# Optimization experiments

Measured on AMD Instinct MI355X. Metric: run time of the kernel, lower is better.

## Reference

```python
import jax, jax.numpy as jnp
import numpy as np

B, C, H, W = 8, 512, 64, 64
CI = C // 8  # inter_channels = 64


def setup_inputs() -> dict:
    key = jax.random.key(0)
    k = jax.random.split(key, 8)
    s = 0.02
    return {
        "x": jax.random.normal(k[0], (B, C, H, W), dtype=jnp.float32),
        "wq": jax.random.normal(k[1], (CI, C), dtype=jnp.float32) * s,
        "bq": jnp.zeros((CI,), dtype=jnp.float32),
        "wk": jax.random.normal(k[2], (CI, C), dtype=jnp.float32) * s,
        "bk": jnp.zeros((CI,), dtype=jnp.float32),
        "wv": jax.random.normal(k[3], (C, C), dtype=jnp.float32) * s,
        "bv": jnp.zeros((C,), dtype=jnp.float32),
        # original inits gamma to 0 (which kills attention branch); use a
        # nonzero value so the attention path contributes to output/grads
        "gamma": jax.random.normal(k[4], (1,), dtype=jnp.float32),
    }


def reference(x, wq, bq, wk, bk, wv, bv, gamma):
    b, c, h, w = x.shape
    n = h * w
    xf = x.reshape(b, c, n)  # (B, C, HW)
    # 1x1 convs == per-pixel linear layers
    q = jnp.einsum("oc,bcn->bon", wq, xf) + bq[None, :, None]  # (B, CI, HW)
    k_ = jnp.einsum("oc,bcn->bon", wk, xf) + bk[None, :, None]  # (B, CI, HW)
    v = jnp.einsum("oc,bcn->bon", wv, xf) + bv[None, :, None]  # (B, C, HW)
    # energy[b, i, j] = <q[:, i], k[:, j]>  -> softmax over j
    energy = jnp.einsum("bdn,bdm->bnm", q, k_)  # (B, HW, HW)
    attn = jax.nn.softmax(energy, axis=-1)
    # note: torch code does bmm(value, attention) -> out[:, c, j] = sum_i v[:, c, i] * attn[:, i, j]
    out = jnp.einsum("bci,bij->bcj", v, attn).reshape(b, c, h, w)
    return gamma[0] * out + x
```

## Files before the change

### kernel.cpp

```cpp
#include <hip/hip_runtime.h>
#include <hip/hip_bf16.h>

#define N_TOK 4096
#define CCH   512

using f32x4  = __attribute__((ext_vector_type(4))) float;
using f32x16 = __attribute__((ext_vector_type(16))) float;
using bf16x4 = __attribute__((ext_vector_type(4))) short;
using bf16x8 = __attribute__((ext_vector_type(8))) short;
using u32x4  = __attribute__((ext_vector_type(4))) unsigned int;

__device__ __forceinline__ short f2bf(float f) {
  __hip_bfloat16 h = __float2bfloat16(f);
  return __builtin_bit_cast(short, h);
}

__device__ __forceinline__ unsigned pkexp(float a, float b) {
  unsigned ua = __builtin_bit_cast(unsigned, __expf(a));
  unsigned ub = __builtin_bit_cast(unsigned, __expf(b));
  ua = ua + 0x7fffu + ((ua >> 16) & 1u);
  ub = ub + 0x7fffu + ((ub >> 16) & 1u);
  return (ua >> 16) | (ub & 0xffff0000u);
}

__device__ __forceinline__ f32x16 mfma32(bf16x8 a, bf16x8 b, f32x16 c) {
  return __builtin_amdgcn_mfma_f32_32x32x16_bf16(a, b, c, 0, 0, 0);
}

__device__ __forceinline__ void gload16(const void* g, void* l) {
  __builtin_amdgcn_global_load_lds(
      (const __attribute__((address_space(1))) void*)g,
      (__attribute__((address_space(3))) void*)l, 16, 0, 0);
}

__device__ __forceinline__ void stage_tile(short* lds, const short* src, int src_stride,
                                           int granules, int tid, int nthr) {
  for (int g = tid; g < granules; g += nthr) {
    int r = g >> 3, c16 = g & 7;
    bf16x8 v = *(const bf16x8*)(src + r * src_stride + c16 * 8);
    *(bf16x8*)(lds + r * 64 + ((c16 ^ (r & 7)) * 8)) = v;
  }
}

__global__ void k_conv_w(const float* wq, const float* wk, const float* wv,
                         const float* bq, const float* bk,
                         short* wqk_bf, short* wv_bf, float* bqk) {
  int idx = blockIdx.x * blockDim.x + threadIdx.x;
  int stride = gridDim.x * blockDim.x;
  const int n1 = 128 * 512;
  const int n2 = 512 * 512;
  for (int i = idx; i < n1; i += stride) {
    int d = i >> 9, c = i & 511;
    float v = (d < 64) ? wq[d * 512 + c] : wk[(d - 64) * 512 + c];
    wqk_bf[i] = f2bf(v);
  }
  for (int i = idx; i < n2; i += stride) wv_bf[i] = f2bf(wv[i]);
  if (idx < 128) bqk[idx] = (idx < 64) ? bq[idx] : bk[idx - 64];
}

__global__ __launch_bounds__(256) void k_transpose_x(const float* __restrict__ x,
                                                     short* __restrict__ xT) {
  __shared__ float tile[64][65];
  const int b = blockIdx.z, c0 = blockIdx.y * 64, n0 = blockIdx.x * 64;
  const int tid = threadIdx.x;
  const int q = tid & 15, r0 = tid >> 4;
#pragma unroll
  for (int p = 0; p < 4; ++p) {
    int c = r0 + p * 16;
    f32x4 v = *(const f32x4*)&x[((long)b * CCH + c0 + c) * N_TOK + n0 + q * 4];
    tile[c][q * 4 + 0] = v[0]; tile[c][q * 4 + 1] = v[1];
    tile[c][q * 4 + 2] = v[2]; tile[c][q * 4 + 3] = v[3];
  }
  __syncthreads();
#pragma unroll
  for (int p = 0; p < 4; ++p) {
    int n = r0 + p * 16;
    bf16x4 o;
    o[0] = f2bf(tile[q * 4 + 0][n]); o[1] = f2bf(tile[q * 4 + 1][n]);
    o[2] = f2bf(tile[q * 4 + 2][n]); o[3] = f2bf(tile[q * 4 + 3][n]);
    *(bf16x4*)&xT[((long)b * N_TOK + n0 + n) * CCH + c0 + q * 4] = o;
  }
}

__global__ __launch_bounds__(512) void k_gemm_qk(
    const short* __restrict__ xT, const short* __restrict__ wqk_bf,
    const float* __restrict__ bqk, short* __restrict__ qkT) {
  __shared__ short An[2][128 * 64];
  __shared__ short Bm[2][128 * 64];
  const int b = blockIdx.z;
  const int n0 = blockIdx.x * 128;
  const int tid = threadIdx.x, lane = tid & 63, w = tid >> 6;
  const int l31 = lane & 31, hi = lane >> 5, x7 = l31 & 7;
  const int nw = w & 3, mw = w >> 2;

  const short* asrc[2];
  const short* bsrc[2];
#pragma unroll
  for (int q = 0; q < 2; ++q) {
    int idx = (w * 2 + q) * 64 + lane;
    int r = idx >> 3, g = idx & 7;
    asrc[q] = xT + ((long long)(b * N_TOK + n0 + r)) * 512 + ((g ^ (r & 7)) * 8);
    bsrc[q] = wqk_bf + (long long)r * 512 + ((g ^ (r & 7)) * 8);
  }
#define STAGEQK(buf, kt)                                           \
  do {                                                             \
    _Pragma("unroll")                                              \
    for (int q = 0; q < 2; ++q) {                                  \
      gload16(asrc[q] + (kt), &An[buf][(w * 2 + q) * 512]);        \
      gload16(bsrc[q] + (kt), &Bm[buf][(w * 2 + q) * 512]);        \
    }                                                              \
  } while (0)

  f32x16 oacc[2] = {};
  STAGEQK(0, 0);
#pragma unroll 1
  for (int t = 0; t < 8; ++t) {
    const int cur = t & 1;
    __syncthreads();
    if (t + 1 < 8) STAGEQK(cur ^ 1, (t + 1) * 64);
#pragma unroll
    for (int ks = 0; ks < 4; ++ks) {
      const int gk = 2 * ks + hi;
      int nrow = nw * 32 + l31;
      bf16x8 anf = *(const bf16x8*)(&An[cur][nrow * 64 + ((gk ^ x7) * 8)]);
#pragma unroll
      for (int mf = 0; mf < 2; ++mf) {
        int mrow = mw * 64 + mf * 32 + l31;
        bf16x8 bmf = *(const bf16x8*)(&Bm[cur][mrow * 64 + ((gk ^ x7) * 8)]);
        oacc[mf] = mfma32(anf, bmf, oacc[mf]);
      }
    }
  }
#undef STAGEQK

#pragma unroll
  for (int mf = 0; mf < 2; ++mf) {
    const int m = mw * 64 + mf * 32 + l31;
    const float bias = bqk[m];
#pragma unroll
    for (int tt = 0; tt < 16; ++tt) {
      int n = n0 + nw * 32 + ((tt & 3) + 8 * (tt >> 2) + 4 * hi);
      qkT[((long long)(b * N_TOK + n)) * 128 + m] = f2bf(oacc[mf][tt] + bias);
    }
  }
}

__global__ __launch_bounds__(256) void k_passA(const short* __restrict__ qkT,
                                               float* __restrict__ Zinv) {
  __shared__ short ql[128 * 64];
  __shared__ short kl[2][128 * 64];
  __shared__ float zbuf[4][128];
  const int b = blockIdx.y, i0 = blockIdx.x * 128;
  const int tid = threadIdx.x, lane = tid & 63, w = tid >> 6;
  const int l31 = lane & 31, hi = lane >> 5;
  const int x7 = l31 & 7;

  stage_tile(ql, qkT + ((long long)b * N_TOK + i0) * 128, 128, 1024, tid, 256);

  const short* ksrc[4];
#pragma unroll
  for (int q = 0; q < 4; ++q) {
    int idx = (w * 4 + q) * 64 + lane;
    int r = idx >> 3, g = idx & 7;
    ksrc[q] = qkT + ((long long)b * N_TOK + r) * 128 + 64 + ((g ^ (r & 7)) * 8);
  }
#define STAGEK(buf, jt)                                              \
  do {                                                               \
    _Pragma("unroll")                                                \
    for (int q = 0; q < 4; ++q)                                      \
      gload16(ksrc[q] + (long long)(jt) * 128 * 128,                 \
              &kl[buf][(w * 4 + q) * 512]);                          \
  } while (0)

  STAGEK(0, 0);
  __syncthreads();

  bf16x8 qfr[4][4];
#pragma unroll
  for (int f = 0; f < 4; ++f)
#pragma unroll
    for (int ks = 0; ks < 4; ++ks)
      qfr[f][ks] = *(const bf16x8*)(&ql[(f * 32 + l31) * 64 + (((2 * ks + hi) ^ x7) * 8)]);

  float zacc[4] = {0.f, 0.f, 0.f, 0.f};
#pragma unroll 1
  for (int jt = 0; jt < 32; ++jt) {
    const int cur = jt & 1;
    if (jt + 1 < 32) STAGEK(cur ^ 1, jt + 1);
    f32x16 sacc[4] = {};
#pragma unroll
    for (int ks = 0; ks < 4; ++ks) {
      bf16x8 kfr = *(const bf16x8*)(&kl[cur][(w * 32 + l31) * 64 + (((2 * ks + hi) ^ x7) * 8)]);
#pragma unroll
      for (int f = 0; f < 4; ++f) sacc[f] = mfma32(kfr, qfr[f][ks], sacc[f]);
    }
#pragma unroll
    for (int f = 0; f < 4; ++f)
#pragma unroll
      for (int t = 0; t < 16; ++t) zacc[f] += __expf(sacc[f][t]);
    __syncthreads();
  }
#undef STAGEK
#pragma unroll
  for (int f = 0; f < 4; ++f) {
    zacc[f] += __shfl_xor(zacc[f], 32, 64);
    if (hi == 0) zbuf[w][f * 32 + l31] = zacc[f];
  }
  __syncthreads();
  if (tid < 128) {
    float z = zbuf[0][tid] + zbuf[1][tid] + zbuf[2][tid] + zbuf[3][tid];
    Zinv[(long long)b * N_TOK + i0 + tid] = 1.0f / z;
  }
}

__global__ __launch_bounds__(512) void k_gemm_v(
    const short* __restrict__ wv_bf, const short* __restrict__ xT,
    const float* __restrict__ bv, const float* __restrict__ Zinv,
    short* __restrict__ v_bf) {
  __shared__ short Ab[2][256 * 64];
  __shared__ short Bb[2][256 * 64];
  const int b = blockIdx.z;
  const int n0 = blockIdx.x * 256, m0 = blockIdx.y * 256;
  const int tid = threadIdx.x;
  const int lane = tid & 63, w = tid >> 6;
  const int l31 = lane & 31, hi = lane >> 5;
  const int x7 = l31 & 7;
  const int mw = w >> 2, nw = w & 3;

  const short* asrc[4];
  const short* bsrc[4];
#pragma unroll
  for (int q = 0; q < 4; ++q) {
    int idx = (w * 4 + q) * 64 + lane;
    int r = idx >> 3, g = idx & 7;
    asrc[q] = wv_bf + (long long)(m0 + r) * 512 + ((g ^ (r & 7)) * 8);
    bsrc[q] = xT + ((long long)(b * N_TOK + n0 + r)) * 512 + ((g ^ (r & 7)) * 8);
  }
#define STAGEV(buf, kt)                                                   \
  do {                                                                    \
    _Pragma("unroll")                                                     \
    for (int q = 0; q < 4; ++q) {                                         \
      gload16(asrc[q] + (kt), &Ab[buf][(w * 4 + q) * 512]);               \
      gload16(bsrc[q] + (kt), &Bb[buf][(w * 4 + q) * 512]);               \
    }                                                                     \
  } while (0)

  f32x16 oacc[4][2] = {};
  STAGEV(0, 0);
#pragma unroll 1
  for (int t = 0; t < 8; ++t) {
    const int cur = t & 1;
    __syncthreads();
    if (t + 1 < 8) STAGEV(cur ^ 1, (t + 1) * 64);
#pragma unroll
    for (int ks = 0; ks < 4; ++ks) {
      const int gk = 2 * ks + hi;
      bf16x8 afr[4], bfr[2];
#pragma unroll
      for (int mf = 0; mf < 4; ++mf) {
        int row = mw * 128 + mf * 32 + l31;
        afr[mf] = *(const bf16x8*)(&Ab[cur][row * 64 + ((gk ^ x7) * 8)]);
      }
#pragma unroll
      for (int nf = 0; nf < 2; ++nf) {
        int row = nw * 64 + nf * 32 + l31;
        bfr[nf] = *(const bf16x8*)(&Bb[cur][row * 64 + ((gk ^ x7) * 8)]);
      }
#pragma unroll
      for (int mf = 0; mf < 4; ++mf)
#pragma unroll
        for (int nf = 0; nf < 2; ++nf)
          oacc[mf][nf] = mfma32(afr[mf], bfr[nf], oacc[mf][nf]);
    }
  }
#undef STAGEV

#pragma unroll
  for (int nf = 0; nf < 2; ++nf) {
    const int n = n0 + nw * 64 + nf * 32 + l31;
    const float zi = Zinv[(long long)b * N_TOK + n];
#pragma unroll
    for (int mf = 0; mf < 4; ++mf)
#pragma unroll
      for (int tt = 0; tt < 16; ++tt) {
        int m = m0 + mw * 128 + mf * 32 + ((tt & 3) + 8 * (tt >> 2) + 4 * hi);
        float v = (oacc[mf][nf][tt] + bv[m]) * zi;
        v_bf[((long long)(b * CCH + m)) * N_TOK + n] = f2bf(v);
      }
  }
}

__global__ __launch_bounds__(512, 2) void k_passB(
    const short* __restrict__ qkT, const short* __restrict__ v_bf,
    const float* __restrict__ x, const float* __restrict__ gamma_p,
    float* __restrict__ out) {
  __shared__ short ql[3][64 * 64];
  __shared__ short vl[3][256 * 64];
  const int b = blockIdx.z;
  const int j0 = blockIdx.x * 256;
  const int c0 = blockIdx.y * 256;
  const int tid = threadIdx.x;
  const int lane = tid & 63, w = tid >> 6;
  const int l31 = lane & 31, hi = lane >> 5;
  const int x7 = l31 & 7;
  const float gamma = *gamma_p;

  bf16x8 kf[4];
  {
    const short* kp = qkT + ((long long)b * N_TOK + j0 + w * 32 + l31) * 128 + 64 + hi * 8;
#pragma unroll
    for (int ks = 0; ks < 4; ++ks) kf[ks] = *(const bf16x8*)(kp + ks * 16);
  }

  const int qidx = w * 64 + lane;
  const int qr = qidx >> 3, qg = qidx & 7;
  const short* qsrc0 = qkT + ((long long)b * N_TOK + qr) * 128 + ((qg ^ (qr & 7)) * 8);
  const short* vsrc0[4];
#pragma unroll
  for (int q = 0; q < 4; ++q) {
    int idx = (w * 4 + q) * 64 + lane;
    int r = idx >> 3, g = idx & 7;
    vsrc0[q] = v_bf + ((long long)(b * CCH + c0 + r)) * N_TOK + ((g ^ (r & 7)) * 8);
  }

  f32x16 oacc[8] = {};

#define STAGE(buf, step)                                              \
  do {                                                                \
    gload16(qsrc0 + (long long)(step) * 64 * 128, &ql[buf][w * 512]); \
    _Pragma("unroll")                                                 \
    for (int q = 0; q < 4; ++q)                                       \
      gload16(vsrc0[q] + (step) * 64, &vl[buf][(w * 4 + q) * 512]);   \
  } while (0)

#define STEP(t, BUF)                                                          \
  do {                                                                        \
    if ((t) < 62) { asm volatile("s_waitcnt vmcnt(5)" ::: "memory"); }        \
    else          { asm volatile("s_waitcnt vmcnt(0)" ::: "memory"); }        \
    __builtin_amdgcn_s_barrier();                                             \
    asm volatile("" ::: "memory");                                            \
    __builtin_amdgcn_sched_barrier(0);                                        \
    if ((t) < 62) STAGE((BUF + 2) % 3, (t) + 2);                              \
    f32x16 sacc[2] = {};                                                      \
    _Pragma("unroll")                                                         \
    for (int ks = 0; ks < 4; ++ks) {                                          \
      int gq = ks * 2 + hi;                                                   \
      bf16x8 qf0 = *(const bf16x8*)(&ql[BUF][l31 * 64 + ((gq ^ x7) * 8)]);    \
      bf16x8 qf1 = *(const bf16x8*)(&ql[BUF][(32 + l31) * 64 + ((gq ^ x7) * 8)]); \
      sacc[0] = mfma32(qf0, kf[ks], sacc[0]);                                 \
      sacc[1] = mfma32(qf1, kf[ks], sacc[1]);                                 \
    }                                                                         \
    bf16x8 pb[4];                                                             \
    _Pragma("unroll")                                                         \
    for (int ks = 0; ks < 4; ++ks) {                                          \
      const int f = ks >> 1, kb = ks & 1;                                     \
      unsigned A0 = pkexp(sacc[f][8 * kb + 0], sacc[f][8 * kb + 1]);          \
      unsigned A1 = pkexp(sacc[f][8 * kb + 2], sacc[f][8 * kb + 3]);          \
      unsigned B0 = pkexp(sacc[f][8 * kb + 4], sacc[f][8 * kb + 5]);          \
      unsigned B1 = pkexp(sacc[f][8 * kb + 6], sacc[f][8 * kb + 7]);          \
      unsigned s0 = __shfl_xor(hi ? A0 : B0, 32, 64);                         \
      unsigned s1 = __shfl_xor(hi ? A1 : B1, 32, 64);                         \
      u32x4 wd = {hi ? s0 : A0, hi ? s1 : A1, hi ? B0 : s0, hi ? B1 : s1};    \
      pb[ks] = __builtin_bit_cast(bf16x8, wd);                                \
    }                                                                         \
    __builtin_amdgcn_s_setprio(1);                                            \
    _Pragma("unroll")                                                         \
    for (int ks = 0; ks < 4; ++ks) {                                          \
      const int gk = 2 * ks + hi;                                             \
      _Pragma("unroll")                                                       \
      for (int cf = 0; cf < 8; ++cf) {                                        \
        bf16x8 vf = *(const bf16x8*)(&vl[BUF][(cf * 32 + l31) * 64 + ((gk ^ x7) * 8)]); \
        oacc[cf] = mfma32(vf, pb[ks], oacc[cf]);                              \
      }                                                                       \
    }                                                                         \
    __builtin_amdgcn_s_setprio(0);                                            \
  } while (0)

  STAGE(0, 0);
  STAGE(1, 1);

#pragma unroll 1
  for (int t0 = 0; t0 < 63; t0 += 3) {
    STEP(t0 + 0, 0);
    STEP(t0 + 1, 1);
    STEP(t0 + 2, 2);
  }
  STEP(63, 0);
#undef STEP
#undef STAGE

  const float* xb = x + (long long)b * CCH * N_TOK;
  float* ob = out + (long long)b * CCH * N_TOK;
  const int j = j0 + w * 32 + l31;
#pragma unroll
  for (int cf = 0; cf < 8; ++cf)
#pragma unroll
    for (int tt = 0; tt < 16; ++tt) {
      int c = c0 + cf * 32 + ((tt & 3) + 8 * (tt >> 2) + 4 * hi);
      long long idx = (long long)c * N_TOK + j;
      ob[idx] = gamma * oacc[cf][tt] + xb[idx];
    }
}

extern "C" void kernel_launch(void* const* d_in, const int* in_sizes, int n_in,
                              void* d_out, int out_size, void* d_ws, size_t ws_size,
                              hipStream_t stream) {
  const float* x     = (const float*)d_in[0];
  const float* wq    = (const float*)d_in[1];
  const float* bq    = (const float*)d_in[2];
  const float* wk    = (const float*)d_in[3];
  const float* bk    = (const float*)d_in[4];
  const float* wv    = (const float*)d_in[5];
  const float* bv    = (const float*)d_in[6];
  const float* gamma = (const float*)d_in[7];
  float* out = (float*)d_out;
  char* ws = (char*)d_ws;

  short* xT     = (short*)(ws);
  short* qkT    = (short*)(ws + 33554432);
  short* v_bf   = (short*)(ws + 41943040);
  float* Zinv   = (float*)(ws + 75497472);
  short* wqk_bf = (short*)(ws + 75628544);
  short* wv_bf  = (short*)(ws + 75759616);
  float* bqk    = (float*)(ws + 76283904);

  k_conv_w<<<dim3(256), dim3(256), 0, stream>>>(wq, wk, wv, bq, bk, wqk_bf, wv_bf, bqk);
  k_transpose_x<<<dim3(64, 8, 8), dim3(256), 0, stream>>>(x, xT);
  k_gemm_qk<<<dim3(32, 1, 8), dim3(512), 0, stream>>>(xT, wqk_bf, bqk, qkT);
  k_passA<<<dim3(32, 8), dim3(256), 0, stream>>>(qkT, Zinv);
  k_gemm_v<<<dim3(16, 2, 8), dim3(512), 0, stream>>>(wv_bf, xT, bv, Zinv, v_bf);
  k_passB<<<dim3(16, 2, 8), dim3(512), 0, stream>>>(qkT, v_bf, x, gamma, out);
}
```

Measured before the change: 285.0 us.

## Retile passB warps into a 2x4 grid over channels and tokens

Each of the 8 warps used to own 32 output tokens across all 256 channels. Now warps form a 2x4 grid: each owns 128 channels by 64 tokens. This halves the V-fragment LDS reads per MFMA, since each V fragment feeds two MFMAs. The cost is that every warp recomputes the QK^T scores and exp for 64 tokens, so score MFMAs and exp work per warp double, and 2x redundant softmax work is spread across the channel halves.

```diff
diff --git a/kernel.cpp b/kernel.cpp
--- a/kernel.cpp
+++ b/kernel.cpp
@@ -303,13 +303,16 @@
   const int lane = tid & 63, w = tid >> 6;
   const int l31 = lane & 31, hi = lane >> 5;
   const int x7 = l31 & 7;
+  const int wc = w >> 2, wj = w & 3;
   const float gamma = *gamma_p;
 
-  bf16x8 kf[4];
-  {
-    const short* kp = qkT + ((long long)b * N_TOK + j0 + w * 32 + l31) * 128 + 64 + hi * 8;
-#pragma unroll
-    for (int ks = 0; ks < 4; ++ks) kf[ks] = *(const bf16x8*)(kp + ks * 16);
+  bf16x8 kf[2][4];
+#pragma unroll
+  for (int js = 0; js < 2; ++js) {
+    const short* kp =
+        qkT + ((long long)b * N_TOK + j0 + wj * 64 + js * 32 + l31) * 128 + 64 + hi * 8;
+#pragma unroll
+    for (int ks = 0; ks < 4; ++ks) kf[js][ks] = *(const bf16x8*)(kp + ks * 16);
   }
 
   const int qidx = w * 64 + lane;
@@ -323,7 +326,7 @@
     vsrc0[q] = v_bf + ((long long)(b * CCH + c0 + r)) * N_TOK + ((g ^ (r & 7)) * 8);
   }
 
-  f32x16 oacc[8] = {};
+  f32x16 oacc[4][2] = {};
 
 #define STAGE(buf, step)                                              \
   do {                                                                \
@@ -341,36 +344,42 @@
     asm volatile("" ::: "memory");                                            \
     __builtin_amdgcn_sched_barrier(0);                                        \
     if ((t) < 62) STAGE((BUF + 2) % 3, (t) + 2);                              \
-    f32x16 sacc[2] = {};                                                      \
+    bf16x8 pb[2][4];                                                          \
     _Pragma("unroll")                                                         \
-    for (int ks = 0; ks < 4; ++ks) {                                          \
-      int gq = ks * 2 + hi;                                                   \
-      bf16x8 qf0 = *(const bf16x8*)(&ql[BUF][l31 * 64 + ((gq ^ x7) * 8)]);    \
-      bf16x8 qf1 = *(const bf16x8*)(&ql[BUF][(32 + l31) * 64 + ((gq ^ x7) * 8)]); \
-      sacc[0] = mfma32(qf0, kf[ks], sacc[0]);                                 \
-      sacc[1] = mfma32(qf1, kf[ks], sacc[1]);                                 \
-    }                                                                         \
-    bf16x8 pb[4];                                                             \
-    _Pragma("unroll")                                                         \
-    for (int ks = 0; ks < 4; ++ks) {                                          \
-      const int f = ks >> 1, kb = ks & 1;                                     \
-      unsigned A0 = pkexp(sacc[f][8 * kb + 0], sacc[f][8 * kb + 1]);          \
-      unsigned A1 = pkexp(sacc[f][8 * kb + 2], sacc[f][8 * kb + 3]);          \
-      unsigned B0 = pkexp(sacc[f][8 * kb + 4], sacc[f][8 * kb + 5]);          \
-      unsigned B1 = pkexp(sacc[f][8 * kb + 6], sacc[f][8 * kb + 7]);          \
-      unsigned s0 = __shfl_xor(hi ? A0 : B0, 32, 64);                         \
-      unsigned s1 = __shfl_xor(hi ? A1 : B1, 32, 64);                         \
-      u32x4 wd = {hi ? s0 : A0, hi ? s1 : A1, hi ? B0 : s0, hi ? B1 : s1};    \
-      pb[ks] = __builtin_bit_cast(bf16x8, wd);                                \
+    for (int js = 0; js < 2; ++js) {                                          \
+      _Pragma("unroll")                                                       \
+      for (int ib = 0; ib < 2; ++ib) {                                        \
+        f32x16 sacc = {};                                                     \
+        _Pragma("unroll")                                                     \
+        for (int ks = 0; ks < 4; ++ks) {                                      \
+          int gq = ks * 2 + hi;                                               \
+          bf16x8 qf =                                                         \
+              *(const bf16x8*)(&ql[BUF][(ib * 32 + l31) * 64 + ((gq ^ x7) * 8)]); \
+          sacc = mfma32(qf, kf[js][ks], sacc);                                \
+        }                                                                     \
+        _Pragma("unroll")                                                     \
+        for (int kb = 0; kb < 2; ++kb) {                                      \
+          unsigned A0 = pkexp(sacc[8 * kb + 0], sacc[8 * kb + 1]);            \
+          unsigned A1 = pkexp(sacc[8 * kb + 2], sacc[8 * kb + 3]);            \
+          unsigned B0 = pkexp(sacc[8 * kb + 4], sacc[8 * kb + 5]);            \
+          unsigned B1 = pkexp(sacc[8 * kb + 6], sacc[8 * kb + 7]);            \
+          unsigned s0 = __shfl_xor(hi ? A0 : B0, 32, 64);                     \
+          unsigned s1 = __shfl_xor(hi ? A1 : B1, 32, 64);                     \
+          u32x4 wd = {hi ? s0 : A0, hi ? s1 : A1, hi ? B0 : s0, hi ? B1 : s1}; \
+          pb[js][2 * ib + kb] = __builtin_bit_cast(bf16x8, wd);               \
+        }                                                                     \
+      }                                                                       \
     }                                                                         \
     __builtin_amdgcn_s_setprio(1);                                            \
     _Pragma("unroll")                                                         \
     for (int ks = 0; ks < 4; ++ks) {                                          \
       const int gk = 2 * ks + hi;                                             \
       _Pragma("unroll")                                                       \
-      for (int cf = 0; cf < 8; ++cf) {                                        \
-        bf16x8 vf = *(const bf16x8*)(&vl[BUF][(cf * 32 + l31) * 64 + ((gk ^ x7) * 8)]); \
-        oacc[cf] = mfma32(vf, pb[ks], oacc[cf]);                              \
+      for (int cs = 0; cs < 4; ++cs) {                                        \
+        bf16x8 vf = *(const bf16x8*)(&vl[BUF][(wc * 128 + cs * 32 + l31) * 64 + \
+                                              ((gk ^ x7) * 8)]);              \
+        oacc[cs][0] = mfma32(vf, pb[0][ks], oacc[cs][0]);                     \
+        oacc[cs][1] = mfma32(vf, pb[1][ks], oacc[cs][1]);                     \
       }                                                                       \
     }                                                                         \
     __builtin_amdgcn_s_setprio(0);                                            \
@@ -391,14 +400,17 @@
 
   const float* xb = x + (long long)b * CCH * N_TOK;
   float* ob = out + (long long)b * CCH * N_TOK;
-  const int j = j0 + w * 32 + l31;
-#pragma unroll
-  for (int cf = 0; cf < 8; ++cf)
-#pragma unroll
-    for (int tt = 0; tt < 16; ++tt) {
-      int c = c0 + cf * 32 + ((tt & 3) + 8 * (tt >> 2) + 4 * hi);
-      long long idx = (long long)c * N_TOK + j;
-      ob[idx] = gamma * oacc[cf][tt] + xb[idx];
+#pragma unroll
+  for (int cs = 0; cs < 4; ++cs)
+#pragma unroll
+    for (int js = 0; js < 2; ++js) {
+      const int j = j0 + wj * 64 + js * 32 + l31;
+#pragma unroll
+      for (int tt = 0; tt < 16; ++tt) {
+        int c = c0 + wc * 128 + cs * 32 + ((tt & 3) + 8 * (tt >> 2) + 4 * hi);
+        long long idx = (long long)c * N_TOK + j;
+        ob[idx] = gamma * oacc[cs][js][tt] + xb[idx];
+      }
     }
 }
 
```

Result: slower. 344.0 us (+20.7%).
